# Optimization experiments

Measured on AMD Instinct MI355X. Metric: run time of the kernel, lower is better.

The kernel has to match this reference:

```python
import jax, jax.numpy as jnp
import numpy as np

P_L = P_R = P_T = P_D = 1  # lrtd_pad = 1
N_BATCH, C, H, W = 2, 64, 256, 256


def _pad_cube(x):
    """x: [6, C, H, W], face order: front, right, back, left, top, down.
    Returns [6, C, H+p_t+p_d, W+p_l+p_r]."""
    p_l, p_r, p_t, p_d = P_L, P_R, P_T, P_D
    f_front, f_right, f_back, f_left, f_top, f_down = (x[i] for i in range(6))
    T = lambda a: jnp.transpose(a, (0, 2, 1))  # swap last two dims of [C,*,*]

    # top plate: [6, C, p_t, W]
    t = jnp.stack([
        f_top[:, -p_t:, :],
        jnp.flip(T(f_top[:, :, -p_t:]), 2),
        jnp.flip(f_top[:, :p_t, :], 2),
        jnp.flip(T(f_top[:, :, :p_t]), 1),
        jnp.flip(f_back[:, :p_t, :], (1, 2)),
        f_front[:, -p_t:, :],
    ], 0)
    # down plate: [6, C, p_d, W]
    d = jnp.stack([
        f_down[:, :p_d, :],
        jnp.flip(T(f_down[:, :, -p_d:]), 1),
        jnp.flip(f_down[:, -p_d:, :], (1, 2)),
        jnp.flip(T(f_down[:, :, :p_d]), 2),
        f_front[:, :p_d, :],
        jnp.flip(f_back[:, -p_d:, :], (1, 2)),
    ], 0)
    # left plate: [6, C, H, p_l]
    l = jnp.stack([
        f_left[:, :, -p_l:],
        f_front[:, :, -p_l:],
        f_right[:, :, -p_l:],
        f_back[:, :, -p_l:],
        T(f_left[:, :p_l, :]),
        jnp.flip(T(f_left[:, -p_l:, :]), 1),
    ], 0)
    # right plate: [6, C, H, p_r]
    r = jnp.stack([
        f_right[:, :, :p_r],
        f_back[:, :, :p_r],
        f_left[:, :, :p_r],
        f_front[:, :, :p_r],
        jnp.flip(T(f_right[:, :p_r, :]), 1),
        T(jnp.flip(f_right[:, -p_r:, :], 1)),
    ], 0)

    def edge(td, lr):  # corner construction (make_cubepad_edge)
        tdp, lrp = td.shape[2], lr.shape[3]
        if tdp > lrp:
            return jnp.tile(lr, (1, 1, tdp, 1))
        return jnp.tile(td, (1, 1, 1, lrp))

    p_tr = edge(t[:, :, -p_t:, -1:], r[:, :, :1, :p_r])
    p_tl = edge(t[:, :, :p_t, :1], l[:, :, :1, :p_l])
    p_dr = edge(d[:, :, -p_d:, -1:], r[:, :, -1:, -p_r:])
    p_dl = edge(d[:, :, :p_d, :1], l[:, :, -1:, -p_l:])

    lcol = jnp.concatenate([p_tl, l, p_dl], 2)   # [6, C, H+p_t+p_d, p_l]
    rcol = jnp.concatenate([p_tr, r, p_dr], 2)   # [6, C, H+p_t+p_d, p_r]
    mid = jnp.concatenate([t, x, d], 2)          # [6, C, H+p_t+p_d, W]
    return jnp.concatenate([lcol, mid, rcol], 3)


def setup_inputs() -> dict:
    key = jax.random.key(0)
    x = jax.random.normal(key, (6 * N_BATCH, C, H, W), dtype=jnp.float32)
    return {"x": x}


def reference(x) -> jnp.ndarray:
    n = x.shape[0] // 6
    xb = x.reshape(n, 6, *x.shape[1:])
    out = jax.vmap(_pad_cube)(xb)  # [N, 6, C, H', W']
    return out.reshape(n * 6, *out.shape[2:])
```

## Files before the change

kernel.cpp:

```cpp
#include <hip/hip_runtime.h>


#define C_  64
#define H_  256
#define W_  256
#define HP  258
#define WP  258
#define FACE_STRIDE (C_ * H_ * W_)
#define PLANE_IN  (H_ * W_)
#define PLANE_OUT (HP * WP)
#define P4_PER_PLANE (PLANE_OUT / 4)

typedef float f4  __attribute__((ext_vector_type(4)));
typedef float f4u __attribute__((ext_vector_type(4), aligned(4)));

__device__ __forceinline__ float value_at(const float* __restrict__ base,
                                          int face, int h, int w) {
#define IN(f, hh, ww) base[(size_t)(f) * FACE_STRIDE + (hh) * W_ + (ww)]
  if (h >= 1 && h <= H_ && w >= 1 && w <= W_) return IN(face, h - 1, w - 1);
  if (h == 0) {
    int wi = w - 1; wi = wi < 0 ? 0 : (wi > 255 ? 255 : wi);
    switch (face) {
      case 0:  return IN(4, 255, wi);
      case 1:  return IN(4, 255 - wi, 255);
      case 2:  return IN(4, 0, 255 - wi);
      case 3:  return IN(4, wi, 0);
      case 4:  return IN(2, 0, 255 - wi);
      default: return IN(0, 255, wi);
    }
  }
  if (h == HP - 1) {
    int wi = w - 1; wi = wi < 0 ? 0 : (wi > 255 ? 255 : wi);
    switch (face) {
      case 0:  return IN(5, 0, wi);
      case 1:  return IN(5, wi, 255);
      case 2:  return IN(5, 255, 255 - wi);
      case 3:  return IN(5, 255 - wi, 0);
      case 4:  return IN(0, 0, wi);
      default: return IN(2, 255, 255 - wi);
    }
  }
  int hi = h - 1;
  if (w == 0) {
    switch (face) {
      case 0:  return IN(3, hi, 255);
      case 1:  return IN(0, hi, 255);
      case 2:  return IN(1, hi, 255);
      case 3:  return IN(2, hi, 255);
      case 4:  return IN(3, 0, hi);
      default: return IN(3, 255, 255 - hi);
    }
  }
  switch (face) {
    case 0:  return IN(1, hi, 0);
    case 1:  return IN(2, hi, 0);
    case 2:  return IN(3, hi, 0);
    case 3:  return IN(0, hi, 0);
    case 4:  return IN(1, 0, 255 - hi);
    default: return IN(1, 255, hi);
  }
#undef IN
}

__global__ void cubepad_v4_kernel(const float* __restrict__ x,
                                  float* __restrict__ out) {
  int p4 = blockIdx.x * blockDim.x + threadIdx.x;
  if (p4 >= P4_PER_PLANE) return;
  const int fgc = blockIdx.y;
  const int fg  = fgc >> 6;
  const int c   = fgc & 63;
  const int face = fg < 6 ? fg : fg - 6;
  const int nb   = fg < 6 ? 0 : 1;
  const float* base = x + (size_t)nb * 6 * FACE_STRIDE + (size_t)c * PLANE_IN;

  const unsigned p = (unsigned)p4 << 2;
  const unsigned h = p / WP;
  const unsigned w = p - h * WP;

  f4 v;
  if (h >= 1u && h <= 256u && w >= 1u && w <= 253u) {
    v = *(const f4u*)(base + (size_t)face * FACE_STRIDE +
                      (size_t)(h - 1) * W_ + (w - 1));
  } else {
#pragma unroll
    for (int e = 0; e < 4; ++e) {
      unsigned pe = p + e;
      unsigned he = pe / WP;
      unsigned we = pe - he * WP;
      v[e] = value_at(base, face, (int)he, (int)we);
    }
  }
  *(f4*)(out + (size_t)fgc * PLANE_OUT + p) = v;
}

extern "C" void kernel_launch(void* const* d_in, const int* in_sizes, int n_in,
                              void* d_out, int out_size, void* d_ws, size_t ws_size,
                              hipStream_t stream) {
  const float* x = (const float*)d_in[0];
  float* out = (float*)d_out;
  dim3 grid((P4_PER_PLANE + 255) / 256, 768);
  cubepad_v4_kernel<<<grid, 256, 0, stream>>>(x, out);
}
```

Before: 339.4 us.

## Batch four unconditional clamped vector loads per thread with nontemporal stores

```diff
diff --git a/kernel.cpp b/kernel.cpp
--- a/kernel.cpp
+++ b/kernel.cpp
@@ -10,6 +10,7 @@
 #define PLANE_IN  (H_ * W_)
 #define PLANE_OUT (HP * WP)
 #define P4_PER_PLANE (PLANE_OUT / 4)
+#define TOTAL_IN (12 * FACE_STRIDE)
 
 typedef float f4  __attribute__((ext_vector_type(4)));
 typedef float f4u __attribute__((ext_vector_type(4), aligned(4)));
@@ -62,35 +63,55 @@
 #undef IN
 }
 
-__global__ void cubepad_v4_kernel(const float* __restrict__ x,
-                                  float* __restrict__ out) {
-  int p4 = blockIdx.x * blockDim.x + threadIdx.x;
-  if (p4 >= P4_PER_PLANE) return;
+__global__ void cubepad_v4x4_kernel(const float* __restrict__ x,
+                                    float* __restrict__ out) {
+  const int t   = threadIdx.x;
   const int fgc = blockIdx.y;
   const int fg  = fgc >> 6;
   const int c   = fgc & 63;
   const int face = fg < 6 ? fg : fg - 6;
   const int nb   = fg < 6 ? 0 : 1;
-  const float* base = x + (size_t)nb * 6 * FACE_STRIDE + (size_t)c * PLANE_IN;
+  const int base_off = nb * 6 * FACE_STRIDE + c * PLANE_IN;
+  const float* base = x + base_off;
 
-  const unsigned p = (unsigned)p4 << 2;
-  const unsigned h = p / WP;
-  const unsigned w = p - h * WP;
+  const int q0 = blockIdx.x * 1024 + t;
 
-  f4 v;
-  if (h >= 1u && h <= 256u && w >= 1u && w <= 253u) {
-    v = *(const f4u*)(base + (size_t)face * FACE_STRIDE +
-                      (size_t)(h - 1) * W_ + (w - 1));
-  } else {
+  f4 v[4];
 #pragma unroll
-    for (int e = 0; e < 4; ++e) {
-      unsigned pe = p + e;
-      unsigned he = pe / WP;
-      unsigned we = pe - he * WP;
-      v[e] = value_at(base, face, (int)he, (int)we);
+  for (int k = 0; k < 4; ++k) {
+    const int p4 = q0 + (k << 8);
+    const unsigned p = (unsigned)p4 << 2;
+    const unsigned h = p / WP;
+    const unsigned w = p - h * WP;
+    int off = base_off + face * FACE_STRIDE + ((int)h - 1) * W_ + ((int)w - 1);
+    off = off < 0 ? 0 : off;
+    off = off > (TOTAL_IN - 4) ? (TOTAL_IN - 4) : off;
+    v[k] = *(const f4u*)(x + off);
+  }
+#pragma unroll
+  for (int k = 0; k < 4; ++k) {
+    const int p4 = q0 + (k << 8);
+    const unsigned p = (unsigned)p4 << 2;
+    const unsigned h = p / WP;
+    const unsigned w = p - h * WP;
+    const bool fast = (h >= 1u) & (h <= 256u) & (w >= 1u) & (w <= 253u);
+    if (p4 < P4_PER_PLANE && !fast) {
+#pragma unroll
+      for (int e = 0; e < 4; ++e) {
+        const unsigned pe = p + e;
+        const unsigned he = pe / WP;
+        const unsigned we = pe - he * WP;
+        v[k][e] = value_at(base, face, (int)he, (int)we);
+      }
     }
   }
-  *(f4*)(out + (size_t)fgc * PLANE_OUT + p) = v;
+  float* oplane = out + (size_t)fgc * PLANE_OUT;
+#pragma unroll
+  for (int k = 0; k < 4; ++k) {
+    const int p4 = q0 + (k << 8);
+    if (p4 < P4_PER_PLANE)
+      __builtin_nontemporal_store(v[k], (f4*)(oplane + ((size_t)p4 << 2)));
+  }
 }
 
 extern "C" void kernel_launch(void* const* d_in, const int* in_sizes, int n_in,
@@ -98,6 +119,6 @@
                               hipStream_t stream) {
   const float* x = (const float*)d_in[0];
   float* out = (float*)d_out;
-  dim3 grid((P4_PER_PLANE + 255) / 256, 768);
-  cubepad_v4_kernel<<<grid, 256, 0, stream>>>(x, out);
+  dim3 grid((P4_PER_PLANE + 1023) / 1024, 768);
+  cubepad_v4x4_kernel<<<grid, 256, 0, stream>>>(x, out);
 }
```

Result: no change. 343.2 us (+1.1%).

## Split interior and border quads into separate blocks with eight quads per thread

Applied to the files above, without the earlier changes.

```diff
diff --git a/kernel.cpp b/kernel.cpp
--- a/kernel.cpp
+++ b/kernel.cpp
@@ -9,7 +9,8 @@
 #define FACE_STRIDE (C_ * H_ * W_)
 #define PLANE_IN  (H_ * W_)
 #define PLANE_OUT (HP * WP)
-#define P4_PER_PLANE (PLANE_OUT / 4)
+#define QP_PLANE  (PLANE_OUT / 4)
+#define TOTAL_IN  (12 * FACE_STRIDE)
 
 typedef float f4  __attribute__((ext_vector_type(4)));
 typedef float f4u __attribute__((ext_vector_type(4), aligned(4)));
@@ -62,35 +63,68 @@
 #undef IN
 }
 
-__global__ void cubepad_v4_kernel(const float* __restrict__ x,
-                                  float* __restrict__ out) {
-  int p4 = blockIdx.x * blockDim.x + threadIdx.x;
-  if (p4 >= P4_PER_PLANE) return;
+__global__ void cubepad_split_kernel(const float* __restrict__ x,
+                                     float* __restrict__ out) {
   const int fgc = blockIdx.y;
   const int fg  = fgc >> 6;
   const int c   = fgc & 63;
   const int face = fg < 6 ? fg : fg - 6;
   const int nb   = fg < 6 ? 0 : 1;
-  const float* base = x + (size_t)nb * 6 * FACE_STRIDE + (size_t)c * PLANE_IN;
+  const int base_off = nb * 6 * FACE_STRIDE + c * PLANE_IN;
+  const float* base = x + base_off;
+  float* oplane = out + (size_t)fgc * PLANE_OUT;
 
-  const unsigned p = (unsigned)p4 << 2;
-  const unsigned h = p / WP;
-  const unsigned w = p - h * WP;
-
-  f4 v;
-  if (h >= 1u && h <= 256u && w >= 1u && w <= 253u) {
-    v = *(const f4u*)(base + (size_t)face * FACE_STRIDE +
-                      (size_t)(h - 1) * W_ + (w - 1));
+  if (blockIdx.x < 9) {
+    const int q0 = blockIdx.x * 2048 + threadIdx.x;
+    f4 v[8];
+    unsigned hh[8], ww[8];
+#pragma unroll
+    for (int k = 0; k < 8; ++k) {
+      const int q = q0 + (k << 8);
+      const unsigned p = (unsigned)q << 2;
+      const unsigned h = p / 258u;
+      const unsigned w = p - h * 258u;
+      hh[k] = h; ww[k] = w;
+      int off = base_off + face * FACE_STRIDE + ((int)h - 1) * W_ + ((int)w - 1);
+      off = off < 0 ? 0 : off;
+      off = off > (TOTAL_IN - 4) ? (TOTAL_IN - 4) : off;
+      v[k] = *(const f4u*)(x + off);
+    }
+#pragma unroll
+    for (int k = 0; k < 8; ++k) {
+      const int q = q0 + (k << 8);
+      const bool pure = (hh[k] >= 1u) & (hh[k] <= 256u) &
+                        (ww[k] >= 1u) & (ww[k] <= 253u) & (q < QP_PLANE);
+      if (pure) *(f4*)(oplane + ((size_t)q << 2)) = v[k];
+    }
   } else {
+    for (int it = 0; it < 3; ++it) {
+      const int j = threadIdx.x + (it << 8);
+      int Q = -1;
+      if (j < 65) {
+        Q = j;
+      } else if (j < 130) {
+        Q = 16576 + (j - 65);
+      } else if (j < 640) {
+        const int jj = j - 130;
+        const int r = 2 + (jj >> 1);
+        const int s = 258 * r;
+        if ((jj & 1) == 0)       Q = (s - 1) >> 2;
+        else if ((s & 3) == 0)   Q = s >> 2;
+      }
+      if (Q >= 0) {
+        f4 v;
 #pragma unroll
-    for (int e = 0; e < 4; ++e) {
-      unsigned pe = p + e;
-      unsigned he = pe / WP;
-      unsigned we = pe - he * WP;
-      v[e] = value_at(base, face, (int)he, (int)we);
+        for (int e = 0; e < 4; ++e) {
+          const unsigned pe = ((unsigned)Q << 2) + e;
+          const unsigned he = pe / 258u;
+          const unsigned we = pe - he * 258u;
+          v[e] = value_at(base, face, (int)he, (int)we);
+        }
+        *(f4*)(oplane + ((size_t)Q << 2)) = v;
+      }
     }
   }
-  *(f4*)(out + (size_t)fgc * PLANE_OUT + p) = v;
 }
 
 extern "C" void kernel_launch(void* const* d_in, const int* in_sizes, int n_in,
@@ -98,6 +132,6 @@
                               hipStream_t stream) {
   const float* x = (const float*)d_in[0];
   float* out = (float*)d_out;
-  dim3 grid((P4_PER_PLANE + 255) / 256, 768);
-  cubepad_v4_kernel<<<grid, 256, 0, stream>>>(x, out);
+  dim3 grid(10, 768);
+  cubepad_split_kernel<<<grid, 256, 0, stream>>>(x, out);
 }
```

New measurement: 368.3 us. +8.5%, slower.

## Stage padded row bands through LDS for aligned vector loads and stores

Applied to the files above, without the earlier changes.

```diff
diff --git a/kernel.cpp b/kernel.cpp
--- a/kernel.cpp
+++ b/kernel.cpp
@@ -9,10 +9,9 @@
 #define FACE_STRIDE (C_ * H_ * W_)
 #define PLANE_IN  (H_ * W_)
 #define PLANE_OUT (HP * WP)
-#define P4_PER_PLANE (PLANE_OUT / 4)
+#define RPB 16
 
-typedef float f4  __attribute__((ext_vector_type(4)));
-typedef float f4u __attribute__((ext_vector_type(4), aligned(4)));
+typedef float f4 __attribute__((ext_vector_type(4)));
 
 __device__ __forceinline__ float value_at(const float* __restrict__ base,
                                           int face, int h, int w) {
@@ -62,35 +61,54 @@
 #undef IN
 }
 
-__global__ void cubepad_v4_kernel(const float* __restrict__ x,
-                                  float* __restrict__ out) {
-  int p4 = blockIdx.x * blockDim.x + threadIdx.x;
-  if (p4 >= P4_PER_PLANE) return;
+__global__ __launch_bounds__(256) void cubepad_lds_kernel(
+    const float* __restrict__ x, float* __restrict__ out) {
+  __shared__ float lds[RPB * WP];
+  const int t   = threadIdx.x;
   const int fgc = blockIdx.y;
   const int fg  = fgc >> 6;
   const int c   = fgc & 63;
   const int face = fg < 6 ? fg : fg - 6;
   const int nb   = fg < 6 ? 0 : 1;
-  const float* base = x + (size_t)nb * 6 * FACE_STRIDE + (size_t)c * PLANE_IN;
+  const float* base = x + (size_t)(nb * 6) * FACE_STRIDE + (size_t)c * PLANE_IN;
 
-  const unsigned p = (unsigned)p4 << 2;
-  const unsigned h = p / WP;
-  const unsigned w = p - h * WP;
+  const int h0    = blockIdx.x * RPB;
+  const int nrows = (h0 == 256) ? 2 : RPB;
 
-  f4 v;
-  if (h >= 1u && h <= 256u && w >= 1u && w <= 253u) {
-    v = *(const f4u*)(base + (size_t)face * FACE_STRIDE +
-                      (size_t)(h - 1) * W_ + (w - 1));
-  } else {
 #pragma unroll
-    for (int e = 0; e < 4; ++e) {
-      unsigned pe = p + e;
-      unsigned he = pe / WP;
-      unsigned we = pe - he * WP;
-      v[e] = value_at(base, face, (int)he, (int)we);
+  for (int j = 0; j < 4; ++j) {
+    const int idx = t + (j << 8);
+    const int r   = idx >> 6;
+    const int qw  = idx & 63;
+    const int h   = h0 + r;
+    if (r < nrows && h >= 1 && h <= 256) {
+      const float* src = base + (size_t)face * FACE_STRIDE +
+                         (size_t)(h - 1) * W_ + (qw << 2);
+      f4 v = *(const f4*)src;
+      float* dst = &lds[r * WP + 1 + (qw << 2)];
+      dst[0] = v.x; dst[1] = v.y; dst[2] = v.z; dst[3] = v.w;
     }
   }
-  *(f4*)(out + (size_t)fgc * PLANE_OUT + p) = v;
+  if (t < 2 * RPB) {
+    const int r = t >> 1, side = t & 1;
+    const int h = h0 + r;
+    if (r < nrows && h >= 1 && h <= 256) {
+      const int w = side ? 257 : 0;
+      lds[r * WP + w] = value_at(base, face, h, w);
+    }
+  }
+  if (h0 == 0) {
+    for (int w = t; w < WP; w += 256) lds[w] = value_at(base, face, 0, w);
+  }
+  if (h0 == 256) {
+    for (int w = t; w < WP; w += 256) lds[WP + w] = value_at(base, face, 257, w);
+  }
+  __syncthreads();
+
+  const int nq = (nrows * WP) >> 2;
+  f4* oq = (f4*)(out + (size_t)fgc * PLANE_OUT + (size_t)h0 * WP);
+  const f4* lq = (const f4*)lds;
+  for (int qi = t; qi < nq; qi += 256) oq[qi] = lq[qi];
 }
 
 extern "C" void kernel_launch(void* const* d_in, const int* in_sizes, int n_in,
@@ -98,6 +116,6 @@
                               hipStream_t stream) {
   const float* x = (const float*)d_in[0];
   float* out = (float*)d_out;
-  dim3 grid((P4_PER_PLANE + 255) / 256, 768);
-  cubepad_v4_kernel<<<grid, 256, 0, stream>>>(x, out);
+  dim3 grid(17, 768);
+  cubepad_lds_kernel<<<grid, 256, 0, stream>>>(x, out);
 }
```

Measured after the change: 339.0 us. About the same (-0.1%).
